# Kernel tuning notes

Hardware: AMD Instinct MI355X
Metric: run time of the kernel (lower is better)

Reference implementation:

```python
import jax, jax.numpy as jnp
import numpy as np

NH = 8       # num attention heads (hardcoded in module)
NL = 6       # n_layers
EPS = 1e-5   # LayerNorm eps (torch default)


def pos_enc(dim, length):
    # faithful to module's positional_encoding: even cols sin, odd cols cos,
    # with angle = pos / 10000^(2i/dim) where i indexes ALL columns via arange(0,2*dim,2)/dim
    pos = jnp.arange(length, dtype=jnp.float32)[:, None]
    div = 1.0 / (10000.0 ** (jnp.arange(0, 2 * dim, 2, dtype=jnp.float32) / dim))
    ang = pos * div[None, :]  # [length, dim]
    cols = jnp.arange(dim)
    return jnp.where(cols % 2 == 0, jnp.sin(ang), jnp.cos(ang))


def layernorm(x):
    m = x.mean(-1, keepdims=True)
    v = x.var(-1, keepdims=True)  # biased, matches torch LayerNorm
    return (x - m) / jnp.sqrt(v + EPS)


def setup_inputs() -> dict:
    key = jax.random.key(0)
    ks = jax.random.split(key, 8)
    S, H = 2048, 1024
    D = H // NH
    sc = 1.0 / np.sqrt(H)  # ~ torch Linear init scale
    return {
        "inputs": jax.random.normal(ks[0], (S, H), jnp.float32),
        "Wq": jax.random.normal(ks[1], (NH, H, D), jnp.float32) * sc,
        "bq": jnp.zeros((NH, D), jnp.float32),
        "Wk": jax.random.normal(ks[2], (NH, H, D), jnp.float32) * sc,
        "bk": jnp.zeros((NH, D), jnp.float32),
        "Wv": jax.random.normal(ks[3], (NH, H, D), jnp.float32) * sc,
        "bv": jnp.zeros((NH, D), jnp.float32),
        "W1": jax.random.normal(ks[4], (H, H), jnp.float32) * sc,
        "b1": jnp.zeros((H,), jnp.float32),
        "W2": jax.random.normal(ks[5], (H, H), jnp.float32) * sc,
        "b2": jnp.zeros((H,), jnp.float32),
    }


def reference(inputs, Wq, bq, Wk, bk, Wv, bv, W1, b1, W2, b2):
    S, H = inputs.shape
    scale = jnp.sqrt(jnp.float32(H))  # module scales by sqrt(hidden), not sqrt(head_dim)
    x = inputs + pos_enc(H, S)        # [S, H]
    kv = x  # dropout in eval mode = identity; k_v_input fixed to layer-0 input (faithful)
    # K/V are identical every layer (shared weights + fixed kv input)
    K = jnp.einsum('sh,nhd->nsd', kv, Wk) + bk[:, None, :]  # [NH, S, D]
    V = jnp.einsum('sh,nhd->nsd', kv, Wv) + bv[:, None, :]
    t_in = x
    for _ in range(NL):
        Q = jnp.einsum('sh,nhd->nsd', t_in, Wq) + bq[:, None, :]
        A = jax.nn.softmax(jnp.einsum('nsd,ntd->nst', Q, K) / scale, axis=-1)
        ctx = jnp.einsum('nst,ntd->nsd', A, V)        # [NH, S, D]
        cat = ctx.transpose(1, 0, 2).reshape(S, H)    # concat heads on feature dim
        mh = layernorm(t_in + cat)
        ff = jax.nn.relu(mh @ W1 + b1) @ W2 + b2
        t_in = layernorm(mh + ff)
    return t_in
```

## Files before the change

kernel.cpp:

```cpp
#include <hip/hip_runtime.h>

#define S_LEN 2048
#define H_DIM 1024
#define NHEAD 8
#define D_HEAD 128
#define KSPLIT 4
#define KV_PER (S_LEN / KSPLIT)

typedef __bf16 bf16x8 __attribute__((ext_vector_type(8)));
typedef float floatx4 __attribute__((ext_vector_type(4)));

__device__ __forceinline__ float b2f(unsigned short u) {
    union { unsigned int i; float f; } v;
    v.i = ((unsigned int)u) << 16;
    return v.f;
}
__device__ __forceinline__ unsigned short f2b(float f) {
    union { float f; unsigned int i; } v;
    v.f = f;
    return (unsigned short)((v.i + 0x7fffu + ((v.i >> 16) & 1u)) >> 16);
}

__device__ __forceinline__ void dma16(void* lds, const void* g) {
    __builtin_amdgcn_global_load_lds(
        (const __attribute__((address_space(1))) void*)g,
        (__attribute__((address_space(3))) void*)lds, 16, 0, 0);
}

__global__ __launch_bounds__(256) void posenc_kernel(
    const float* __restrict__ in, float* __restrict__ xf,
    unsigned short* __restrict__ xb)
{
    int g = blockIdx.x * 256 + threadIdx.x;
    int s = g >> 10;
    int h = g & 1023;
    float dv = powf(10000.0f, -(float)h * (1.0f / 512.0f));
    float ang = (float)s * dv;
    float pe = (h & 1) ? cosf(ang) : sinf(ang);
    float x = in[g] + pe;
    xf[g] = x;
    xb[g] = f2b(x);
}

__global__ __launch_bounds__(256) void transpose_all(
    const float* __restrict__ Wq, const float* __restrict__ Wk,
    const float* __restrict__ Wv, const float* __restrict__ W1,
    const float* __restrict__ W2,
    unsigned short* __restrict__ WqT, unsigned short* __restrict__ WkT,
    unsigned short* __restrict__ WvT, unsigned short* __restrict__ W1T,
    unsigned short* __restrict__ W2T)
{
    __shared__ unsigned short tile[32][33];
    const int z = blockIdx.z;
    const float* ih;
    unsigned short* oh;
    int ldin;
    if (z < 8)       { ih = Wq + (size_t)z * 131072;        oh = WqT + (size_t)z * 131072;        ldin = 128; }
    else if (z < 16) { ih = Wk + (size_t)(z - 8) * 131072;  oh = WkT + (size_t)(z - 8) * 131072;  ldin = 128; }
    else if (z < 24) { ih = Wv + (size_t)(z - 16) * 131072; oh = WvT + (size_t)(z - 16) * 131072; ldin = 128; }
    else if (z < 32) { ih = W1 + (size_t)(z - 24) * 128;    oh = W1T + (size_t)(z - 24) * 131072; ldin = 1024; }
    else             { ih = W2 + (size_t)(z - 32) * 128;    oh = W2T + (size_t)(z - 32) * 131072; ldin = 1024; }
    const int r0 = blockIdx.y * 32, c0 = blockIdx.x * 32;
    const int tx = threadIdx.x, ty = threadIdx.y;
    for (int i = ty; i < 32; i += 8)
        tile[i][tx] = f2b(ih[(size_t)(r0 + i) * ldin + c0 + tx]);
    __syncthreads();
    for (int i = ty; i < 32; i += 8)
        oh[(size_t)(c0 + i) * 1024 + r0 + tx] = tile[tx][i];
}

template <int MODE, bool RELU>
__device__ __forceinline__ void gemm_core(
    unsigned short* sA0, unsigned short* sB0,
    const unsigned short* A, const unsigned short* Bt,
    const float* bias, float* Cf, unsigned short* Cb,
    int N, int K, int ldt, int i0, int j0)
{
    const int tid = threadIdx.x;
    const int wave = tid >> 6, lane = tid & 63;
    const int quad = lane >> 4, l16 = lane & 15;
    const int wm = (wave >> 1) * 32, wn = (wave & 1) * 32;

    const int srow = lane >> 3;
    const int schunk = (lane & 7) ^ (srow & 7);
    const unsigned short* Ap0 = A + (size_t)(i0 + wave * 8 + srow) * K + schunk * 8;
    const unsigned short* Ap1 = A + (size_t)(i0 + 32 + wave * 8 + srow) * K + schunk * 8;
    const unsigned short* Bp0 = Bt + (size_t)(j0 + wave * 8 + srow) * K + schunk * 8;
    const unsigned short* Bp1 = Bt + (size_t)(j0 + 32 + wave * 8 + srow) * K + schunk * 8;
    const int ld0 = (wave * 8) * 64, ld1 = (32 + wave * 8) * 64;

    floatx4 z4 = {0.f, 0.f, 0.f, 0.f};
    floatx4 acc[2][2];
#pragma unroll
    for (int i = 0; i < 2; i++)
#pragma unroll
        for (int j = 0; j < 2; j++) acc[i][j] = z4;

    dma16(sA0 + ld0, Ap0);
    dma16(sA0 + ld1, Ap1);
    dma16(sB0 + ld0, Bp0);
    dma16(sB0 + ld1, Bp1);
    __syncthreads();

    int buf = 0;
    for (int k0 = 0; k0 < K; k0 += 64) {
        if (k0 + 64 < K) {
            unsigned short* nA = sA0 + (buf ^ 1) * 4096;
            unsigned short* nB = sB0 + (buf ^ 1) * 4096;
            dma16(nA + ld0, Ap0 + k0 + 64);
            dma16(nA + ld1, Ap1 + k0 + 64);
            dma16(nB + ld0, Bp0 + k0 + 64);
            dma16(nB + ld1, Bp1 + k0 + 64);
        }
        const unsigned short* cA = sA0 + buf * 4096;
        const unsigned short* cB = sB0 + buf * 4096;
#pragma unroll
        for (int kh = 0; kh < 2; kh++) {
            bf16x8 af[2], bfr[2];
#pragma unroll
            for (int mi = 0; mi < 2; mi++) {
                int row = wm + mi * 16 + l16;
                int p = (kh * 4 + quad) ^ (l16 & 7);
                af[mi] = *(const bf16x8*)(cA + row * 64 + p * 8);
            }
#pragma unroll
            for (int ni = 0; ni < 2; ni++) {
                int row = wn + ni * 16 + l16;
                int p = (kh * 4 + quad) ^ (l16 & 7);
                bfr[ni] = *(const bf16x8*)(cB + row * 64 + p * 8);
            }
#pragma unroll
            for (int mi = 0; mi < 2; mi++)
#pragma unroll
                for (int ni = 0; ni < 2; ni++)
                    acc[mi][ni] = __builtin_amdgcn_mfma_f32_16x16x32_bf16(
                        af[mi], bfr[ni], acc[mi][ni], 0, 0, 0);
        }
        __syncthreads();
        buf ^= 1;
    }

#pragma unroll
    for (int mi = 0; mi < 2; mi++) {
#pragma unroll
        for (int ni = 0; ni < 2; ni++) {
            const int col = j0 + wn + ni * 16 + l16;
            const float bval = bias[col];
#pragma unroll
            for (int r = 0; r < 4; r++) {
                const int row_o = i0 + wm + mi * 16 + quad * 4 + r;
                float v = acc[mi][ni][r] + bval;
                if (RELU) v = fmaxf(v, 0.0f);
                if (MODE == 0) Cb[(size_t)row_o * N + col] = f2b(v);
                else if (MODE == 1) Cb[(size_t)col * ldt + row_o] = f2b(v);
                else Cf[(size_t)row_o * N + col] = v;
            }
        }
    }
}

template <int MODE, bool RELU>
__global__ __launch_bounds__(256, 4) void gemm_bt(
    const unsigned short* __restrict__ A, const unsigned short* __restrict__ Bt,
    const float* __restrict__ bias, float* __restrict__ Cf,
    unsigned short* __restrict__ Cb, int M, int N, int K, int ldt)
{
    __shared__ __align__(16) unsigned short sA[2 * 64 * 64];
    __shared__ __align__(16) unsigned short sB[2 * 64 * 64];
    gemm_core<MODE, RELU>(sA, sB, A, Bt, bias, Cf, Cb, N, K, ldt,
                          blockIdx.y * 64, blockIdx.x * 64);
}

__global__ __launch_bounds__(256, 4) void gemm_kv(
    const unsigned short* __restrict__ A,
    const unsigned short* __restrict__ WkT, const unsigned short* __restrict__ WvT,
    const float* __restrict__ bk, const float* __restrict__ bv,
    unsigned short* __restrict__ Kb, unsigned short* __restrict__ Vtb)
{
    __shared__ __align__(16) unsigned short sA[2 * 64 * 64];
    __shared__ __align__(16) unsigned short sB[2 * 64 * 64];
    if (blockIdx.z == 0)
        gemm_core<0, false>(sA, sB, A, WkT, bk, nullptr, Kb, H_DIM, H_DIM, 0,
                            blockIdx.y * 64, blockIdx.x * 64);
    else
        gemm_core<1, false>(sA, sB, A, WvT, bv, nullptr, Vtb, H_DIM, H_DIM, S_LEN,
                            blockIdx.y * 64, blockIdx.x * 64);
}

__global__ __launch_bounds__(256, 2) void flash_attn(
    const unsigned short* __restrict__ Qg, const unsigned short* __restrict__ Kg,
    const unsigned short* __restrict__ Vt, unsigned short* __restrict__ Op,
    float* __restrict__ Lp)
{
    extern __shared__ __align__(16) unsigned short smem[];
    unsigned short* sK0 = smem;
    unsigned short* sV0 = smem + 16384;
    unsigned short* sP = smem + 32768;

    const int tid = threadIdx.x;
    const int wave = tid >> 6, lane = tid & 63;
    const int quad = lane >> 4, l16 = lane & 15;
    const int head = blockIdx.y;
    const int q0 = blockIdx.x * 64;
    const int split = blockIdx.z;
    const int h0 = head * D_HEAD;

    bf16x8 aq[4];
    const int qrow = q0 + wave * 16 + l16;
#pragma unroll
    for (int ks = 0; ks < 4; ks++)
        aq[ks] = *(const bf16x8*)(Qg + (size_t)qrow * H_DIM + h0 + ks * 32 + quad * 8);

    unsigned short* myP = sP + wave * (16 * 72);

    const int k_r = wave * 4 + (lane >> 4);
    const int k_c = (lane & 15) ^ (k_r & 15);
    const int v_r = wave * 8 + (lane >> 3);
    const int v_c = (lane & 7) ^ (v_r & 7);

    const unsigned short* Kbase = Kg + h0;
    const unsigned short* Vbase = Vt + (size_t)h0 * S_LEN;
    const int kt0 = split * KV_PER;

    floatx4 z4 = {0.f, 0.f, 0.f, 0.f};
    floatx4 o[8];
#pragma unroll
    for (int i = 0; i < 8; i++) o[i] = z4;
    float l_r[4] = {0.f, 0.f, 0.f, 0.f};

#pragma unroll
    for (int it = 0; it < 4; it++) {
        dma16(sK0 + (wave * 4 + it * 16) * 128,
              Kbase + (size_t)(kt0 + k_r + it * 16) * H_DIM + k_c * 8);
        dma16(sV0 + (wave * 8 + it * 32) * 64,
              Vbase + (size_t)(v_r + it * 32) * S_LEN + kt0 + v_c * 8);
    }
    __syncthreads();

    int buf = 0;
    for (int it0 = 0; it0 < KV_PER; it0 += 64) {
        const int t0 = kt0 + it0;
        if (it0 + 64 < KV_PER) {
            const int nt = t0 + 64;
            unsigned short* nK = sK0 + (buf ^ 1) * 8192;
            unsigned short* nV = sV0 + (buf ^ 1) * 8192;
#pragma unroll
            for (int it = 0; it < 4; it++) {
                dma16(nK + (wave * 4 + it * 16) * 128,
                      Kbase + (size_t)(nt + k_r + it * 16) * H_DIM + k_c * 8);
                dma16(nV + (wave * 8 + it * 32) * 64,
                      Vbase + (size_t)(v_r + it * 32) * S_LEN + nt + v_c * 8);
            }
        }
        const unsigned short* cK = sK0 + buf * 8192;
        const unsigned short* cV = sV0 + buf * 8192;

        floatx4 sc[4];
#pragma unroll
        for (int ni = 0; ni < 4; ni++) {
            sc[ni] = z4;
#pragma unroll
            for (int ks = 0; ks < 4; ks++) {
                int p = (ks * 4 + quad) ^ l16;
                bf16x8 bk = *(const bf16x8*)(cK + (ni * 16 + l16) * 128 + p * 8);
                sc[ni] = __builtin_amdgcn_mfma_f32_16x16x32_bf16(aq[ks], bk, sc[ni], 0, 0, 0);
            }
        }

#pragma unroll
        for (int ni = 0; ni < 4; ni++)
#pragma unroll
            for (int r = 0; r < 4; r++) {
                float p = __expf(sc[ni][r] * 0.03125f);
                sc[ni][r] = p;
                l_r[r] += p;
            }

#pragma unroll
        for (int ni = 0; ni < 4; ni++)
#pragma unroll
            for (int r = 0; r < 4; r++) {
                int prow = quad * 4 + r;
                myP[prow * 72 + ((ni * 16 + l16) ^ ((prow & 8) << 1))] = f2b(sc[ni][r]);
            }
        bf16x8 ap[2];
#pragma unroll
        for (int ks = 0; ks < 2; ks++)
            ap[ks] = *(const bf16x8*)(myP + l16 * 72 + ((ks * 32 + quad * 8) ^ ((l16 & 8) << 1)));

#pragma unroll
        for (int ni = 0; ni < 8; ni++) {
#pragma unroll
            for (int ks = 0; ks < 2; ks++) {
                int p = (ks * 4 + quad) ^ (l16 & 7);
                bf16x8 bv = *(const bf16x8*)(cV + (ni * 16 + l16) * 64 + p * 8);
                o[ni] = __builtin_amdgcn_mfma_f32_16x16x32_bf16(ap[ks], bv, o[ni], 0, 0, 0);
            }
        }

        __syncthreads();
        buf ^= 1;
    }

#pragma unroll
    for (int r = 0; r < 4; r++)
#pragma unroll
        for (int off = 1; off < 16; off <<= 1)
            l_r[r] += __shfl_xor(l_r[r], off, 64);

#pragma unroll
    for (int r = 0; r < 4; r++) {
        float inv = 1.0f / l_r[r];
        int row = q0 + wave * 16 + quad * 4 + r;
#pragma unroll
        for (int ni = 0; ni < 8; ni++)
            Op[((size_t)split * S_LEN + row) * H_DIM + h0 + ni * 16 + l16] =
                f2b(o[ni][r] * inv);
        if (l16 == 0)
            Lp[(split * NHEAD + head) * S_LEN + row] = l_r[r];
    }
}

__global__ __launch_bounds__(256) void merge_add_layernorm(
    const float* __restrict__ t, const unsigned short* __restrict__ Op,
    const float* __restrict__ Lp,
    float* __restrict__ of, unsigned short* __restrict__ ob)
{
    __shared__ float red[8];
    const int row = blockIdx.x, tid = threadIdx.x;
    const int head = tid >> 5;
    const size_t base = (size_t)row * H_DIM + tid * 4;

    float l_s[KSPLIT];
    ushort4 os[KSPLIT];
#pragma unroll
    for (int sp = 0; sp < KSPLIT; sp++) {
        os[sp] = *(const ushort4*)(Op + ((size_t)sp * S_LEN + row) * H_DIM + tid * 4);
        l_s[sp] = Lp[(sp * NHEAD + head) * S_LEN + row];
    }
    float W = 0.f, a0 = 0.f, a1 = 0.f, a2 = 0.f, a3 = 0.f;
#pragma unroll
    for (int sp = 0; sp < KSPLIT; sp++) {
        float w = l_s[sp];
        W += w;
        a0 += w * b2f(os[sp].x);
        a1 += w * b2f(os[sp].y);
        a2 += w * b2f(os[sp].z);
        a3 += w * b2f(os[sp].w);
    }
    float inv = 1.0f / W;
    float4 x = *(const float4*)(t + base);
    float v0 = x.x + a0 * inv, v1 = x.y + a1 * inv;
    float v2 = x.z + a2 * inv, v3 = x.w + a3 * inv;

    float s = v0 + v1 + v2 + v3;
    float q = v0 * v0 + v1 * v1 + v2 * v2 + v3 * v3;
#pragma unroll
    for (int off = 32; off >= 1; off >>= 1) {
        s += __shfl_xor(s, off, 64);
        q += __shfl_xor(q, off, 64);
    }
    if ((tid & 63) == 0) { red[tid >> 6] = s; red[4 + (tid >> 6)] = q; }
    __syncthreads();
    s = red[0] + red[1] + red[2] + red[3];
    q = red[4] + red[5] + red[6] + red[7];
    const float mean = s * (1.0f / (float)H_DIM);
    const float var = q * (1.0f / (float)H_DIM) - mean * mean;
    const float rstd = rsqrtf(var + 1e-5f);
    float o0 = (v0 - mean) * rstd, o1 = (v1 - mean) * rstd;
    float o2 = (v2 - mean) * rstd, o3 = (v3 - mean) * rstd;
    *(float4*)(of + base) = make_float4(o0, o1, o2, o3);
    *(ushort4*)(ob + base) = make_ushort4(f2b(o0), f2b(o1), f2b(o2), f2b(o3));
}

__global__ __launch_bounds__(256) void add_layernorm(
    const float* __restrict__ a, const float* __restrict__ b,
    float* __restrict__ of, unsigned short* __restrict__ ob)
{
    __shared__ float red[8];
    const int row = blockIdx.x, tid = threadIdx.x;
    const size_t base = (size_t)row * H_DIM + tid * 4;
    float4 x = *(const float4*)(a + base);
    float4 y = *(const float4*)(b + base);
    float v0 = x.x + y.x, v1 = x.y + y.y, v2 = x.z + y.z, v3 = x.w + y.w;
    float s = v0 + v1 + v2 + v3;
    float q = v0 * v0 + v1 * v1 + v2 * v2 + v3 * v3;
#pragma unroll
    for (int off = 32; off >= 1; off >>= 1) {
        s += __shfl_xor(s, off, 64);
        q += __shfl_xor(q, off, 64);
    }
    if ((tid & 63) == 0) { red[tid >> 6] = s; red[4 + (tid >> 6)] = q; }
    __syncthreads();
    s = red[0] + red[1] + red[2] + red[3];
    q = red[4] + red[5] + red[6] + red[7];
    const float mean = s * (1.0f / (float)H_DIM);
    const float var = q * (1.0f / (float)H_DIM) - mean * mean;
    const float rstd = rsqrtf(var + 1e-5f);
    float o0 = (v0 - mean) * rstd, o1 = (v1 - mean) * rstd;
    float o2 = (v2 - mean) * rstd, o3 = (v3 - mean) * rstd;
    *(float4*)(of + base) = make_float4(o0, o1, o2, o3);
    *(ushort4*)(ob + base) = make_ushort4(f2b(o0), f2b(o1), f2b(o2), f2b(o3));
}

extern "C" void kernel_launch(void* const* d_in, const int* in_sizes, int n_in,
                              void* d_out, int out_size, void* d_ws, size_t ws_size,
                              hipStream_t stream)
{
    (void)in_sizes; (void)n_in; (void)out_size; (void)ws_size;
    const float* in = (const float*)d_in[0];
    const float* Wq = (const float*)d_in[1];
    const float* bq = (const float*)d_in[2];
    const float* Wk = (const float*)d_in[3];
    const float* bk = (const float*)d_in[4];
    const float* Wv = (const float*)d_in[5];
    const float* bv = (const float*)d_in[6];
    const float* W1 = (const float*)d_in[7];
    const float* b1 = (const float*)d_in[8];
    const float* W2 = (const float*)d_in[9];
    const float* b2 = (const float*)d_in[10];

    char* ws = (char*)d_ws;
    const size_t MB = 1024 * 1024;
    float* t_f32 = (float*)(ws + 0 * MB);
    float* cf_f32 = (float*)(ws + 8 * MB);
    unsigned short* t_b = (unsigned short*)(ws + 16 * MB);
    unsigned short* K_b = (unsigned short*)(ws + 20 * MB);
    unsigned short* Vt_b = (unsigned short*)(ws + 24 * MB);
    unsigned short* Q_b = (unsigned short*)(ws + 28 * MB);
    unsigned short* WqT = (unsigned short*)(ws + 32 * MB);
    unsigned short* WkT = (unsigned short*)(ws + 34 * MB);
    unsigned short* WvT = (unsigned short*)(ws + 36 * MB);
    unsigned short* W1T = (unsigned short*)(ws + 38 * MB);
    unsigned short* W2T = (unsigned short*)(ws + 40 * MB);
    unsigned short* Op = (unsigned short*)(ws + 42 * MB);
    float* Lp = (float*)(ws + 58 * MB);

    (void)hipFuncSetAttribute(reinterpret_cast<const void*>(&flash_attn),
                              hipFuncAttributeMaxDynamicSharedMemorySize, 74752);

    transpose_all<<<dim3(4, 32, 40), dim3(32, 8), 0, stream>>>(
        Wq, Wk, Wv, W1, W2, WqT, WkT, WvT, W1T, W2T);

    posenc_kernel<<<(S_LEN * H_DIM) / 256, 256, 0, stream>>>(in, t_f32, t_b);

    dim3 gg(H_DIM / 64, S_LEN / 64);
    gemm_kv<<<dim3(16, 32, 2), 256, 0, stream>>>(t_b, WkT, WvT, bk, bv, K_b, Vt_b);

    for (int layer = 0; layer < 6; layer++) {
        gemm_bt<0, false><<<gg, 256, 0, stream>>>(t_b, WqT, bq, nullptr, Q_b, S_LEN, H_DIM, H_DIM, 0);
        flash_attn<<<dim3(S_LEN / 64, NHEAD, KSPLIT), 256, 74752, stream>>>(Q_b, K_b, Vt_b, Op, Lp);
        merge_add_layernorm<<<S_LEN, 256, 0, stream>>>(t_f32, Op, Lp, t_f32, t_b);
        gemm_bt<0, true><<<gg, 256, 0, stream>>>(t_b, W1T, b1, nullptr, Q_b, S_LEN, H_DIM, H_DIM, 0);
        gemm_bt<2, false><<<gg, 256, 0, stream>>>(Q_b, W2T, b2, cf_f32, nullptr, S_LEN, H_DIM, H_DIM, 0);
        float* of = (layer == 5) ? (float*)d_out : t_f32;
        add_layernorm<<<S_LEN, 256, 0, stream>>>(t_f32, cf_f32, of, t_b);
    }
}
```

Before: 598.0 us.

## Enlarge GEMM tiles to 128x128 and halve attention KV split

```diff
diff --git a/kernel.cpp b/kernel.cpp
--- a/kernel.cpp
+++ b/kernel.cpp
@@ -4,7 +4,7 @@
 #define H_DIM 1024
 #define NHEAD 8
 #define D_HEAD 128
-#define KSPLIT 4
+#define KSPLIT 2
 #define KV_PER (S_LEN / KSPLIT)
 
 typedef __bf16 bf16x8 __attribute__((ext_vector_type(8)));
@@ -70,69 +70,70 @@
 }
 
 template <int MODE, bool RELU>
-__device__ __forceinline__ void gemm_core(
-    unsigned short* sA0, unsigned short* sB0,
+__device__ __forceinline__ void gemm128_core(
+    unsigned short* sA, unsigned short* sB,
     const unsigned short* A, const unsigned short* Bt,
-    const float* bias, float* Cf, unsigned short* Cb,
-    int N, int K, int ldt, int i0, int j0)
-{
+    const float* bias, float* Cf, unsigned short* Cb, int ldt, int i0, int j0)
+{
+    const int K = H_DIM;
     const int tid = threadIdx.x;
     const int wave = tid >> 6, lane = tid & 63;
     const int quad = lane >> 4, l16 = lane & 15;
-    const int wm = (wave >> 1) * 32, wn = (wave & 1) * 32;
+    const int wm = (wave >> 1) * 64, wn = (wave & 1) * 64;
 
     const int srow = lane >> 3;
-    const int schunk = (lane & 7) ^ (srow & 7);
-    const unsigned short* Ap0 = A + (size_t)(i0 + wave * 8 + srow) * K + schunk * 8;
-    const unsigned short* Ap1 = A + (size_t)(i0 + 32 + wave * 8 + srow) * K + schunk * 8;
-    const unsigned short* Bp0 = Bt + (size_t)(j0 + wave * 8 + srow) * K + schunk * 8;
-    const unsigned short* Bp1 = Bt + (size_t)(j0 + 32 + wave * 8 + srow) * K + schunk * 8;
-    const int ld0 = (wave * 8) * 64, ld1 = (32 + wave * 8) * 64;
+    const int schunk = (lane & 7) ^ srow;
+    const unsigned short* Ap = A + (size_t)(i0 + wave * 8 + srow) * K + schunk * 8;
+    const unsigned short* Bp = Bt + (size_t)(j0 + wave * 8 + srow) * K + schunk * 8;
 
     floatx4 z4 = {0.f, 0.f, 0.f, 0.f};
-    floatx4 acc[2][2];
-#pragma unroll
-    for (int i = 0; i < 2; i++)
-#pragma unroll
-        for (int j = 0; j < 2; j++) acc[i][j] = z4;
-
-    dma16(sA0 + ld0, Ap0);
-    dma16(sA0 + ld1, Ap1);
-    dma16(sB0 + ld0, Bp0);
-    dma16(sB0 + ld1, Bp1);
+    floatx4 acc[4][4];
+#pragma unroll
+    for (int i = 0; i < 4; i++)
+#pragma unroll
+        for (int j = 0; j < 4; j++) acc[i][j] = z4;
+
+#pragma unroll
+    for (int it = 0; it < 4; it++) {
+        const int lb = (wave * 8 + it * 32) * 64;
+        dma16(sA + lb, Ap + (size_t)(it * 32) * K);
+        dma16(sB + lb, Bp + (size_t)(it * 32) * K);
+    }
     __syncthreads();
 
     int buf = 0;
     for (int k0 = 0; k0 < K; k0 += 64) {
         if (k0 + 64 < K) {
-            unsigned short* nA = sA0 + (buf ^ 1) * 4096;
-            unsigned short* nB = sB0 + (buf ^ 1) * 4096;
-            dma16(nA + ld0, Ap0 + k0 + 64);
-            dma16(nA + ld1, Ap1 + k0 + 64);
-            dma16(nB + ld0, Bp0 + k0 + 64);
-            dma16(nB + ld1, Bp1 + k0 + 64);
-        }
-        const unsigned short* cA = sA0 + buf * 4096;
-        const unsigned short* cB = sB0 + buf * 4096;
+            unsigned short* nA = sA + (buf ^ 1) * 8192;
+            unsigned short* nB = sB + (buf ^ 1) * 8192;
+#pragma unroll
+            for (int it = 0; it < 4; it++) {
+                const int lb = (wave * 8 + it * 32) * 64;
+                dma16(nA + lb, Ap + (size_t)(it * 32) * K + k0 + 64);
+                dma16(nB + lb, Bp + (size_t)(it * 32) * K + k0 + 64);
+            }
+        }
+        const unsigned short* cA = sA + buf * 8192;
+        const unsigned short* cB = sB + buf * 8192;
 #pragma unroll
         for (int kh = 0; kh < 2; kh++) {
-            bf16x8 af[2], bfr[2];
-#pragma unroll
-            for (int mi = 0; mi < 2; mi++) {
+            bf16x8 af[4], bfr[4];
+#pragma unroll
+            for (int mi = 0; mi < 4; mi++) {
                 int row = wm + mi * 16 + l16;
                 int p = (kh * 4 + quad) ^ (l16 & 7);
                 af[mi] = *(const bf16x8*)(cA + row * 64 + p * 8);
             }
 #pragma unroll
-            for (int ni = 0; ni < 2; ni++) {
+            for (int ni = 0; ni < 4; ni++) {
                 int row = wn + ni * 16 + l16;
                 int p = (kh * 4 + quad) ^ (l16 & 7);
                 bfr[ni] = *(const bf16x8*)(cB + row * 64 + p * 8);
             }
 #pragma unroll
-            for (int mi = 0; mi < 2; mi++)
-#pragma unroll
-                for (int ni = 0; ni < 2; ni++)
+            for (int mi = 0; mi < 4; mi++)
+#pragma unroll
+                for (int ni = 0; ni < 4; ni++)
                     acc[mi][ni] = __builtin_amdgcn_mfma_f32_16x16x32_bf16(
                         af[mi], bfr[ni], acc[mi][ni], 0, 0, 0);
         }
@@ -141,9 +142,9 @@
     }
 
 #pragma unroll
-    for (int mi = 0; mi < 2; mi++) {
-#pragma unroll
-        for (int ni = 0; ni < 2; ni++) {
+    for (int mi = 0; mi < 4; mi++) {
+#pragma unroll
+        for (int ni = 0; ni < 4; ni++) {
             const int col = j0 + wn + ni * 16 + l16;
             const float bval = bias[col];
 #pragma unroll
@@ -151,40 +152,38 @@
                 const int row_o = i0 + wm + mi * 16 + quad * 4 + r;
                 float v = acc[mi][ni][r] + bval;
                 if (RELU) v = fmaxf(v, 0.0f);
-                if (MODE == 0) Cb[(size_t)row_o * N + col] = f2b(v);
+                if (MODE == 0) Cb[(size_t)row_o * H_DIM + col] = f2b(v);
                 else if (MODE == 1) Cb[(size_t)col * ldt + row_o] = f2b(v);
-                else Cf[(size_t)row_o * N + col] = v;
+                else Cf[(size_t)row_o * H_DIM + col] = v;
             }
         }
     }
 }
 
 template <int MODE, bool RELU>
-__global__ __launch_bounds__(256, 4) void gemm_bt(
+__global__ __launch_bounds__(256, 2) void gemm128(
     const unsigned short* __restrict__ A, const unsigned short* __restrict__ Bt,
     const float* __restrict__ bias, float* __restrict__ Cf,
-    unsigned short* __restrict__ Cb, int M, int N, int K, int ldt)
-{
-    __shared__ __align__(16) unsigned short sA[2 * 64 * 64];
-    __shared__ __align__(16) unsigned short sB[2 * 64 * 64];
-    gemm_core<MODE, RELU>(sA, sB, A, Bt, bias, Cf, Cb, N, K, ldt,
-                          blockIdx.y * 64, blockIdx.x * 64);
-}
-
-__global__ __launch_bounds__(256, 4) void gemm_kv(
+    unsigned short* __restrict__ Cb, int ldt)
+{
+    extern __shared__ __align__(16) unsigned short gsm[];
+    gemm128_core<MODE, RELU>(gsm, gsm + 16384, A, Bt, bias, Cf, Cb, ldt,
+                             blockIdx.y * 128, blockIdx.x * 128);
+}
+
+__global__ __launch_bounds__(256, 2) void gemm_kv(
     const unsigned short* __restrict__ A,
     const unsigned short* __restrict__ WkT, const unsigned short* __restrict__ WvT,
     const float* __restrict__ bk, const float* __restrict__ bv,
     unsigned short* __restrict__ Kb, unsigned short* __restrict__ Vtb)
 {
-    __shared__ __align__(16) unsigned short sA[2 * 64 * 64];
-    __shared__ __align__(16) unsigned short sB[2 * 64 * 64];
+    extern __shared__ __align__(16) unsigned short gsm[];
     if (blockIdx.z == 0)
-        gemm_core<0, false>(sA, sB, A, WkT, bk, nullptr, Kb, H_DIM, H_DIM, 0,
-                            blockIdx.y * 64, blockIdx.x * 64);
+        gemm128_core<0, false>(gsm, gsm + 16384, A, WkT, bk, nullptr, Kb, 0,
+                               blockIdx.y * 128, blockIdx.x * 128);
     else
-        gemm_core<1, false>(sA, sB, A, WvT, bv, nullptr, Vtb, H_DIM, H_DIM, S_LEN,
-                            blockIdx.y * 64, blockIdx.x * 64);
+        gemm128_core<1, false>(gsm, gsm + 16384, A, WvT, bv, nullptr, Vtb, S_LEN,
+                               blockIdx.y * 128, blockIdx.x * 128);
 }
 
 __global__ __launch_bounds__(256, 2) void flash_attn(
@@ -438,21 +437,29 @@
 
     (void)hipFuncSetAttribute(reinterpret_cast<const void*>(&flash_attn),
                               hipFuncAttributeMaxDynamicSharedMemorySize, 74752);
+    (void)hipFuncSetAttribute(reinterpret_cast<const void*>(&gemm128<0, false>),
+                              hipFuncAttributeMaxDynamicSharedMemorySize, 65536);
+    (void)hipFuncSetAttribute(reinterpret_cast<const void*>(&gemm128<0, true>),
+                              hipFuncAttributeMaxDynamicSharedMemorySize, 65536);
+    (void)hipFuncSetAttribute(reinterpret_cast<const void*>(&gemm128<2, false>),
+                              hipFuncAttributeMaxDynamicSharedMemorySize, 65536);
+    (void)hipFuncSetAttribute(reinterpret_cast<const void*>(&gemm_kv),
+                              hipFuncAttributeMaxDynamicSharedMemorySize, 65536);
 
     transpose_all<<<dim3(4, 32, 40), dim3(32, 8), 0, stream>>>(
         Wq, Wk, Wv, W1, W2, WqT, WkT, WvT, W1T, W2T);
 
     posenc_kernel<<<(S_LEN * H_DIM) / 256, 256, 0, stream>>>(in, t_f32, t_b);
 
-    dim3 gg(H_DIM / 64, S_LEN / 64);
-    gemm_kv<<<dim3(16, 32, 2), 256, 0, stream>>>(t_b, WkT, WvT, bk, bv, K_b, Vt_b);
+    dim3 gg(H_DIM / 128, S_LEN / 128);
+    gemm_kv<<<dim3(8, 16, 2), 256, 65536, stream>>>(t_b, WkT, WvT, bk, bv, K_b, Vt_b);
 
     for (int layer = 0; layer < 6; layer++) {
-        gemm_bt<0, false><<<gg, 256, 0, stream>>>(t_b, WqT, bq, nullptr, Q_b, S_LEN, H_DIM, H_DIM, 0);
+        gemm128<0, false><<<gg, 256, 65536, stream>>>(t_b, WqT, bq, nullptr, Q_b, 0);
         flash_attn<<<dim3(S_LEN / 64, NHEAD, KSPLIT), 256, 74752, stream>>>(Q_b, K_b, Vt_b, Op, Lp);
         merge_add_layernorm<<<S_LEN, 256, 0, stream>>>(t_f32, Op, Lp, t_f32, t_b);
-        gemm_bt<0, true><<<gg, 256, 0, stream>>>(t_b, W1T, b1, nullptr, Q_b, S_LEN, H_DIM, H_DIM, 0);
-        gemm_bt<2, false><<<gg, 256, 0, stream>>>(Q_b, W2T, b2, cf_f32, nullptr, S_LEN, H_DIM, H_DIM, 0);
+        gemm128<0, true><<<gg, 256, 65536, stream>>>(t_b, W1T, b1, nullptr, Q_b, 0);
+        gemm128<2, false><<<gg, 256, 65536, stream>>>(Q_b, W2T, b2, cf_f32, nullptr, 0);
         float* of = (layer == 5) ? (float*)d_out : t_f32;
         add_layernorm<<<S_LEN, 256, 0, stream>>>(t_f32, cf_f32, of, t_b);
     }
```

Measured after the change: 593.1 us. Within noise of the previous version (-0.8%).
